# Kernel tuning notes

Hardware: AMD Instinct MI355X
Metric: run time of the kernel (lower is better)

The kernel has to match this reference:

```python
import jax, jax.numpy as jnp
import numpy as np

N = 100000      # nodes
E = 1600000     # nnz of precomputed A^K (avg degree 16)
D = 64          # in_feats
C = 64          # n_classes
LN_EPS = 1e-5


def setup_inputs() -> dict:
    key = jax.random.key(0)
    ks = jax.random.split(key, 8)
    feat = jax.random.normal(ks[0], (N, D), dtype=jnp.float32)
    feat_ori = jax.random.normal(ks[1], (N, D), dtype=jnp.float32)
    row = jax.random.randint(ks[2], (E,), 0, N)
    col = jax.random.randint(ks[3], (E,), 0, N)
    adj_vals = jax.random.uniform(ks[4], (E,), dtype=jnp.float32)
    # Linear params (xavier_uniform weight, zero bias)
    limit = float(np.sqrt(6.0 / (D + C)))
    W = jax.random.uniform(ks[5], (C, D), dtype=jnp.float32, minval=-limit, maxval=limit)
    b = jnp.zeros((C,), dtype=jnp.float32)
    # LayerNorm params
    gamma = jnp.ones((C,), dtype=jnp.float32)
    beta = jnp.zeros((C,), dtype=jnp.float32)
    return {"feat": feat, "feat_ori": feat_ori, "row": row, "col": col,
            "adj_vals": adj_vals, "W": W, "b": b, "gamma": gamma, "beta": beta}


def reference(feat, feat_ori, row, col, adj_vals, W, b, gamma, beta):
    # NOTE: in the source, h = (1-alpha)*feat + alpha*feat_ori is dead code
    # (immediately overwritten by the SpMM of raw feat), so it is omitted.
    # SpMM: h[i] = sum_{e: row[e]=i} adj_vals[e] * feat[col[e]]   -> [N, D]
    msgs = adj_vals[:, None] * feat[col]            # [E, D] gather + scale
    h = jax.ops.segment_sum(msgs, row, num_segments=N)  # [N, D] scatter-add
    # Dense Linear: [N, D] @ [D, C] + [C]
    h = jnp.einsum('nd,cd->nc', h, W) + b
    # LayerNorm over last dim
    mu = jnp.mean(h, axis=-1, keepdims=True)
    var = jnp.mean(jnp.square(h - mu), axis=-1, keepdims=True)
    h = (h - mu) * jax.lax.rsqrt(var + LN_EPS) * gamma + beta
    return h
```

## Files before the change

kernel.cpp:

```cpp
#include <hip/hip_runtime.h>


typedef unsigned int u32;
typedef unsigned short u16;
typedef unsigned long long u64;
#define RFL(x) __builtin_amdgcn_readfirstlane(x)

#define EPB 2048
#define MAXBK 2048
#define CAP 2048

__device__ __forceinline__ float bf2f(u16 v) {
    return __uint_as_float((u32)v << 16);
}
__device__ __forceinline__ u16 f2bf(float f) {
    u32 b = __float_as_uint(f);
    return (u16)((b + 0x7FFFu + ((b >> 16) & 1u)) >> 16);
}

__global__ __launch_bounds__(256) void k_bhist(const int* __restrict__ row,
                                               u32* __restrict__ hist2d,
                                               int E, int NBK) {
    __shared__ u32 cnt[MAXBK];
    for (int i = threadIdx.x; i < NBK; i += 256) cnt[i] = 0;
    __syncthreads();
    int e0 = blockIdx.x * EPB;
#pragma unroll
    for (int j = 0; j < EPB / 256; ++j) {
        int e = e0 + j * 256 + threadIdx.x;
        if (e < E) atomicAdd(&cnt[(u32)row[e] >> 6], 1u);
    }
    __syncthreads();
    u32* dst = hist2d + (size_t)blockIdx.x * NBK;
    for (int i = threadIdx.x; i < NBK; i += 256) dst[i] = cnt[i];
}

__device__ __forceinline__ u32 blk_scan256(u32 v, u32* wsum, u32& total) {
    int lane = threadIdx.x & 63, wid = threadIdx.x >> 6;
    u32 incl = v;
#pragma unroll
    for (int o = 1; o < 64; o <<= 1) {
        u32 u = __shfl_up(incl, o);
        if (lane >= o) incl += u;
    }
    if (lane == 63) wsum[wid] = incl;
    __syncthreads();
    u32 woff = 0;
    for (int w = 0; w < wid; ++w) woff += wsum[w];
    total = wsum[0] + wsum[1] + wsum[2] + wsum[3];
    __syncthreads();
    return woff + incl - v;
}

__global__ __launch_bounds__(256) void k_bscan(u32* __restrict__ hist2d,
                                               u32* __restrict__ btot,
                                               int NBLK, int NBK) {
    __shared__ u32 wsum[4];
    int bkt = blockIdx.x;
    u32 carry = 0;
    for (int r = 0; r < NBLK; r += 256) {
        int blk = r + threadIdx.x;
        u32 v = (blk < NBLK) ? hist2d[(size_t)blk * NBK + bkt] : 0;
        u32 tot;
        u32 ex = blk_scan256(v, wsum, tot);
        if (blk < NBLK) hist2d[(size_t)blk * NBK + bkt] = ex + carry;
        carry += tot;
    }
    if (threadIdx.x == 0) btot[bkt] = carry;
}

__global__ __launch_bounds__(256) void k_scanb2(const u32* __restrict__ btot,
                                                u32* __restrict__ bbase,
                                                int NBK, int E) {
    __shared__ u32 wsum[4];
    u32 carry = 0;
    for (int r = 0; r < NBK; r += 256) {
        int i = r + threadIdx.x;
        u32 v = (i < NBK) ? btot[i] : 0;
        u32 tot;
        u32 ex = blk_scan256(v, wsum, tot);
        if (i < NBK) bbase[i] = ex + carry;
        carry += tot;
    }
    if (threadIdx.x == 0) bbase[NBK] = (u32)E;
}

__global__ __launch_bounds__(256) void k_bscat(const int* __restrict__ row,
                                               const int* __restrict__ col,
                                               const float* __restrict__ vals,
                                               const u32* __restrict__ hist2d,
                                               const u32* __restrict__ bbase,
                                               u64* __restrict__ epair1,
                                               int E, int NBK) {
    __shared__ u32 lbase[MAXBK];
    __shared__ u32 lcnt[MAXBK];
    const u32* hrow = hist2d + (size_t)blockIdx.x * NBK;
    for (int i = threadIdx.x; i < NBK; i += 256) {
        lbase[i] = bbase[i] + hrow[i];
        lcnt[i] = 0;
    }
    __syncthreads();
    int e0 = blockIdx.x * EPB;
#pragma unroll
    for (int j = 0; j < EPB / 256; ++j) {
        int e = e0 + j * 256 + threadIdx.x;
        if (e < E) {
            u32 r = (u32)row[e];
            u32 bkt = r >> 6;
            u32 lrank = atomicAdd(&lcnt[bkt], 1u);
            u32 pos = lbase[bkt] + lrank;
            u32 meta = (u32)col[e] | ((r & 63u) << 26);
            epair1[pos] = (u64)meta | ((u64)__float_as_uint(vals[e]) << 32);
        }
    }
}

__global__ __launch_bounds__(256) void k_gemm(const float* __restrict__ feat,
                                              const float* __restrict__ W,
                                              u16* __restrict__ G, int N) {
    __shared__ float fs[4096];
    int lane = threadIdx.x & 63, wid = threadIdx.x >> 6;
    int n0 = blockIdx.x * 64;
    int valid = N - n0; if (valid > 64) valid = 64;
    int elems = valid * 64;
    for (int idx = threadIdx.x * 4; idx < elems; idx += 1024)
        *reinterpret_cast<float4*>(&fs[idx]) =
            *reinterpret_cast<const float4*>(&feat[(size_t)n0 * 64 + idx]);
    float wr[64];
#pragma unroll
    for (int d4 = 0; d4 < 16; ++d4) {
        float4 w4 = *reinterpret_cast<const float4*>(&W[lane * 64 + d4 * 4]);
        wr[d4 * 4 + 0] = w4.x; wr[d4 * 4 + 1] = w4.y;
        wr[d4 * 4 + 2] = w4.z; wr[d4 * 4 + 3] = w4.w;
    }
    __syncthreads();
    for (int j = 0; j < 16; ++j) {
        int r = wid * 16 + j;
        if (r >= valid) break;
        float o = 0.f;
#pragma unroll
        for (int d4 = 0; d4 < 16; ++d4) {
            float4 h4 = *reinterpret_cast<const float4*>(&fs[r * 64 + d4 * 4]);
            o = fmaf(h4.x, wr[d4 * 4 + 0], o);
            o = fmaf(h4.y, wr[d4 * 4 + 1], o);
            o = fmaf(h4.z, wr[d4 * 4 + 2], o);
            o = fmaf(h4.w, wr[d4 * 4 + 3], o);
        }
        G[(size_t)(n0 + r) * 64 + lane] = f2bf(o);
    }
}

__global__ __launch_bounds__(256) void k_node2(
    const u16* __restrict__ G, const u64* __restrict__ epair1,
    const u32* __restrict__ bbase, const float* __restrict__ bias,
    const float* __restrict__ gamma, const float* __restrict__ beta,
    float* __restrict__ out, int N)
{
    __shared__ u64 sp[CAP];
    __shared__ u32 cnt[64], base[64], cnt2[64];
    int tid = threadIdx.x, lane = tid & 63, wid = tid >> 6;
    int bkt = blockIdx.x;
    if (tid < 64) { cnt[tid] = 0; cnt2[tid] = 0; }
    __syncthreads();
    int s = RFL((int)bbase[bkt]);
    int t = RFL((int)bbase[bkt + 1]);
    int m = t - s;
    bool fits = (m <= CAP);

    const u32* meta1 = (const u32*)epair1;
    for (int i = s + tid; i < t; i += 256)
        atomicAdd(&cnt[meta1[2 * (size_t)i] >> 26], 1u);
    __syncthreads();
    if (tid < 64) {
        u32 v = cnt[tid];
        u32 incl = v;
#pragma unroll
        for (int o = 1; o < 64; o <<= 1) {
            u32 u = __shfl_up(incl, o);
            if (tid >= o) incl += u;
        }
        base[tid] = incl - v;
    }
    __syncthreads();
    if (fits) {
        for (int i = s + tid; i < t; i += 256) {
            u64 p = epair1[i];
            u32 mm = (u32)p;
            u32 r = mm >> 26;
            u32 rank = atomicAdd(&cnt2[r], 1u);
            sp[base[r] + rank] = (p & 0xFFFFFFFF00000000ull) | (u64)(mm & 0x03FFFFFFu);
        }
    }
    __syncthreads();

    int rbase = bkt << 6;
    for (int j = 0; j < 16; ++j) {
        int r = wid * 16 + j;
        int n = rbase + r;
        if (n >= N) break;
        float acc0 = 0.f, acc1 = 0.f;
        if (fits) {
            int e0 = base[r], e1 = base[r] + cnt[r];
            int i = e0;
            for (; i + 8 <= e1; i += 8) {
                u64 p0 = sp[i],     p1 = sp[i + 1];
                u64 p2 = sp[i + 2], p3 = sp[i + 3];
                u64 p4 = sp[i + 4], p5 = sp[i + 5];
                u64 p6 = sp[i + 6], p7 = sp[i + 7];
                u32 c0 = RFL((u32)p0), b0 = RFL((u32)(p0 >> 32));
                u32 c1 = RFL((u32)p1), b1 = RFL((u32)(p1 >> 32));
                u32 c2 = RFL((u32)p2), b2 = RFL((u32)(p2 >> 32));
                u32 c3 = RFL((u32)p3), b3 = RFL((u32)(p3 >> 32));
                u32 c4 = RFL((u32)p4), b4 = RFL((u32)(p4 >> 32));
                u32 c5 = RFL((u32)p5), b5 = RFL((u32)(p5 >> 32));
                u32 c6 = RFL((u32)p6), b6 = RFL((u32)(p6 >> 32));
                u32 c7 = RFL((u32)p7), b7 = RFL((u32)(p7 >> 32));
                float g0 = bf2f(G[((size_t)c0 << 6) | lane]);
                float g1 = bf2f(G[((size_t)c1 << 6) | lane]);
                float g2 = bf2f(G[((size_t)c2 << 6) | lane]);
                float g3 = bf2f(G[((size_t)c3 << 6) | lane]);
                float g4 = bf2f(G[((size_t)c4 << 6) | lane]);
                float g5 = bf2f(G[((size_t)c5 << 6) | lane]);
                float g6 = bf2f(G[((size_t)c6 << 6) | lane]);
                float g7 = bf2f(G[((size_t)c7 << 6) | lane]);
                acc0 = fmaf(__uint_as_float(b0), g0, acc0);
                acc1 = fmaf(__uint_as_float(b1), g1, acc1);
                acc0 = fmaf(__uint_as_float(b2), g2, acc0);
                acc1 = fmaf(__uint_as_float(b3), g3, acc1);
                acc0 = fmaf(__uint_as_float(b4), g4, acc0);
                acc1 = fmaf(__uint_as_float(b5), g5, acc1);
                acc0 = fmaf(__uint_as_float(b6), g6, acc0);
                acc1 = fmaf(__uint_as_float(b7), g7, acc1);
            }
            for (; i < e1; ++i) {
                u64 p = sp[i];
                u32 c = RFL((u32)p), b = RFL((u32)(p >> 32));
                acc0 = fmaf(__uint_as_float(b), bf2f(G[((size_t)c << 6) | lane]), acc0);
            }
        } else {
            for (int i = s; i < t; ++i) {
                u64 p = epair1[i];
                u32 mm = RFL((u32)p);
                if ((int)(mm >> 26) == r) {
                    u32 b = RFL((u32)(p >> 32));
                    acc0 = fmaf(__uint_as_float(b),
                                bf2f(G[((size_t)(mm & 0x03FFFFFFu) << 6) | lane]), acc0);
                }
            }
        }
        float o = acc0 + acc1 + bias[lane];

        float ssum = o;
#pragma unroll
        for (int off = 32; off; off >>= 1) ssum += __shfl_xor(ssum, off);
        float mu = ssum * 0.015625f;
        float dv = o - mu;
        float vs = dv * dv;
#pragma unroll
        for (int off = 32; off; off >>= 1) vs += __shfl_xor(vs, off);
        float inv = rsqrtf(vs * 0.015625f + 1e-5f);
        out[((size_t)n << 6) + lane] = dv * inv * gamma[lane] + beta[lane];
    }
}

extern "C" void kernel_launch(void* const* d_in, const int* in_sizes, int n_in,
                              void* d_out, int out_size, void* d_ws, size_t ws_size,
                              hipStream_t stream) {
    const float* feat  = (const float*)d_in[0];
    const int*   row   = (const int*)d_in[2];
    const int*   col   = (const int*)d_in[3];
    const float* vals  = (const float*)d_in[4];
    const float* W     = (const float*)d_in[5];
    const float* bias  = (const float*)d_in[6];
    const float* gamma = (const float*)d_in[7];
    const float* beta  = (const float*)d_in[8];
    float* out = (float*)d_out;

    const int D = 64;
    int N = in_sizes[0] / D;
    int E = in_sizes[2];

    int NBK  = (N + 63) / 64;
    int NBLK = (E + EPB - 1) / EPB;

    char* ws = (char*)d_ws;
    u16*   G      = (u16*)ws;
    u32*   hist2d = (u32*)ws;
    size_t sizeA  = (size_t)N * 128;
    size_t hsize  = (size_t)NBLK * NBK * 4;
    if (hsize > sizeA) sizeA = hsize;
    size_t boffB  = (sizeA + 255) & ~(size_t)255;
    u64*   epair1 = (u64*)(ws + boffB);
    size_t boffC  = boffB + (((size_t)E * 8 + 255) & ~(size_t)255);
    u32*   btot   = (u32*)(ws + boffC);
    u32*   bbase  = btot + NBK;

    k_bhist <<<NBLK, 256, 0, stream>>>(row, hist2d, E, NBK);
    k_bscan <<<NBK, 256, 0, stream>>>(hist2d, btot, NBLK, NBK);
    k_scanb2<<<1, 256, 0, stream>>>(btot, bbase, NBK, E);
    k_bscat <<<NBLK, 256, 0, stream>>>(row, col, vals, hist2d, bbase,
                                       epair1, E, NBK);
    k_gemm  <<<(N + 63) / 64, 256, 0, stream>>>(feat, W, G, N);
    k_node2 <<<NBK, 256, 0, stream>>>(G, epair1, bbase, bias, gamma, beta,
                                      out, N);
}
```

Before: 162.2 us.

## Shrink histogram block count and fuse edge scatter with dense GEMM launch

New measurement: 130.2 us. -19.7%, faster.

```diff
diff --git a/kernel.cpp b/kernel.cpp
--- a/kernel.cpp
+++ b/kernel.cpp
@@ -6,7 +6,7 @@
 typedef unsigned long long u64;
 #define RFL(x) __builtin_amdgcn_readfirstlane(x)
 
-#define EPB 2048
+#define NBLKC 64
 #define MAXBK 2048
 #define CAP 2048
 
@@ -20,19 +20,25 @@
 
 __global__ __launch_bounds__(256) void k_bhist(const int* __restrict__ row,
                                                u32* __restrict__ hist2d,
-                                               int E, int NBK) {
+                                               int E, int NBK, int CH) {
     __shared__ u32 cnt[MAXBK];
-    for (int i = threadIdx.x; i < NBK; i += 256) cnt[i] = 0;
-    __syncthreads();
-    int e0 = blockIdx.x * EPB;
-#pragma unroll
-    for (int j = 0; j < EPB / 256; ++j) {
-        int e = e0 + j * 256 + threadIdx.x;
-        if (e < E) atomicAdd(&cnt[(u32)row[e] >> 6], 1u);
-    }
+    int tid = threadIdx.x;
+    for (int i = tid; i < NBK; i += 256) cnt[i] = 0;
+    __syncthreads();
+    int e0 = blockIdx.x * CH;
+    int e1 = e0 + CH; if (e1 > E) e1 = E;
+    int ev = e1 & ~3;
+    for (int i = e0 + tid * 4; i < ev; i += 1024) {
+        int4 r = *reinterpret_cast<const int4*>(&row[i]);
+        atomicAdd(&cnt[(u32)r.x >> 6], 1u);
+        atomicAdd(&cnt[(u32)r.y >> 6], 1u);
+        atomicAdd(&cnt[(u32)r.z >> 6], 1u);
+        atomicAdd(&cnt[(u32)r.w >> 6], 1u);
+    }
+    { int i = ev + tid; if (i < e1) atomicAdd(&cnt[(u32)row[i] >> 6], 1u); }
     __syncthreads();
     u32* dst = hist2d + (size_t)blockIdx.x * NBK;
-    for (int i = threadIdx.x; i < NBK; i += 256) dst[i] = cnt[i];
+    for (int i = tid; i < NBK; i += 256) dst[i] = cnt[i];
 }
 
 __device__ __forceinline__ u32 blk_scan256(u32 v, u32* wsum, u32& total) {
@@ -85,68 +91,88 @@
     if (threadIdx.x == 0) bbase[NBK] = (u32)E;
 }
 
-__global__ __launch_bounds__(256) void k_bscat(const int* __restrict__ row,
-                                               const int* __restrict__ col,
-                                               const float* __restrict__ vals,
-                                               const u32* __restrict__ hist2d,
-                                               const u32* __restrict__ bbase,
-                                               u64* __restrict__ epair1,
-                                               int E, int NBK) {
-    __shared__ u32 lbase[MAXBK];
-    __shared__ u32 lcnt[MAXBK];
-    const u32* hrow = hist2d + (size_t)blockIdx.x * NBK;
-    for (int i = threadIdx.x; i < NBK; i += 256) {
-        lbase[i] = bbase[i] + hrow[i];
-        lcnt[i] = 0;
-    }
-    __syncthreads();
-    int e0 = blockIdx.x * EPB;
-#pragma unroll
-    for (int j = 0; j < EPB / 256; ++j) {
-        int e = e0 + j * 256 + threadIdx.x;
-        if (e < E) {
-            u32 r = (u32)row[e];
-            u32 bkt = r >> 6;
-            u32 lrank = atomicAdd(&lcnt[bkt], 1u);
-            u32 pos = lbase[bkt] + lrank;
-            u32 meta = (u32)col[e] | ((r & 63u) << 26);
-            epair1[pos] = (u64)meta | ((u64)__float_as_uint(vals[e]) << 32);
-        }
-    }
-}
-
-__global__ __launch_bounds__(256) void k_gemm(const float* __restrict__ feat,
-                                              const float* __restrict__ W,
-                                              u16* __restrict__ G, int N) {
-    __shared__ float fs[4096];
-    int lane = threadIdx.x & 63, wid = threadIdx.x >> 6;
-    int n0 = blockIdx.x * 64;
-    int valid = N - n0; if (valid > 64) valid = 64;
-    int elems = valid * 64;
-    for (int idx = threadIdx.x * 4; idx < elems; idx += 1024)
-        *reinterpret_cast<float4*>(&fs[idx]) =
-            *reinterpret_cast<const float4*>(&feat[(size_t)n0 * 64 + idx]);
-    float wr[64];
-#pragma unroll
-    for (int d4 = 0; d4 < 16; ++d4) {
-        float4 w4 = *reinterpret_cast<const float4*>(&W[lane * 64 + d4 * 4]);
-        wr[d4 * 4 + 0] = w4.x; wr[d4 * 4 + 1] = w4.y;
-        wr[d4 * 4 + 2] = w4.z; wr[d4 * 4 + 3] = w4.w;
-    }
-    __syncthreads();
-    for (int j = 0; j < 16; ++j) {
-        int r = wid * 16 + j;
-        if (r >= valid) break;
-        float o = 0.f;
+__global__ __launch_bounds__(256) void k_scatgemm(
+    const int* __restrict__ row, const int* __restrict__ col,
+    const float* __restrict__ vals, const u32* __restrict__ hist2d,
+    const u32* __restrict__ bbase, u64* __restrict__ epair1,
+    const float* __restrict__ feat, const float* __restrict__ W,
+    u16* __restrict__ G, int E, int N, int NBK, int NBLK, int CH)
+{
+    __shared__ __align__(16) u32 smem[4096];
+    int tid = threadIdx.x;
+    if ((int)blockIdx.x < NBLK) {
+        u32* lbase = smem;
+        u32* lcnt  = smem + NBK;
+        int blk = blockIdx.x;
+        const u32* hrow = hist2d + (size_t)blk * NBK;
+        for (int i = tid; i < NBK; i += 256) {
+            lbase[i] = bbase[i] + hrow[i];
+            lcnt[i] = 0;
+        }
+        __syncthreads();
+        int e0 = blk * CH;
+        int e1 = e0 + CH; if (e1 > E) e1 = E;
+        int ev = e1 & ~3;
+        for (int i = e0 + tid * 4; i < ev; i += 1024) {
+            int4 r = *reinterpret_cast<const int4*>(&row[i]);
+            int4 c = *reinterpret_cast<const int4*>(&col[i]);
+            float4 v = *reinterpret_cast<const float4*>(&vals[i]);
+            u32 k0 = (u32)r.x >> 6, k1 = (u32)r.y >> 6;
+            u32 k2 = (u32)r.z >> 6, k3 = (u32)r.w >> 6;
+            u32 q0 = atomicAdd(&lcnt[k0], 1u);
+            u32 q1 = atomicAdd(&lcnt[k1], 1u);
+            u32 q2 = atomicAdd(&lcnt[k2], 1u);
+            u32 q3 = atomicAdd(&lcnt[k3], 1u);
+            epair1[lbase[k0] + q0] = (u64)((u32)c.x | (((u32)r.x & 63u) << 26))
+                                   | ((u64)__float_as_uint(v.x) << 32);
+            epair1[lbase[k1] + q1] = (u64)((u32)c.y | (((u32)r.y & 63u) << 26))
+                                   | ((u64)__float_as_uint(v.y) << 32);
+            epair1[lbase[k2] + q2] = (u64)((u32)c.z | (((u32)r.z & 63u) << 26))
+                                   | ((u64)__float_as_uint(v.z) << 32);
+            epair1[lbase[k3] + q3] = (u64)((u32)c.w | (((u32)r.w & 63u) << 26))
+                                   | ((u64)__float_as_uint(v.w) << 32);
+        }
+        {
+            int i = ev + tid;
+            if (i < e1) {
+                u32 r = (u32)row[i];
+                u32 k = r >> 6;
+                u32 q = atomicAdd(&lcnt[k], 1u);
+                epair1[lbase[k] + q] = (u64)((u32)col[i] | ((r & 63u) << 26))
+                                     | ((u64)__float_as_uint(vals[i]) << 32);
+            }
+        }
+    } else {
+        float* fs = (float*)smem;
+        int lane = tid & 63, wid = tid >> 6;
+        int n0 = ((int)blockIdx.x - NBLK) * 64;
+        int valid = N - n0; if (valid > 64) valid = 64;
+        int elems = valid * 64;
+        for (int idx = tid * 4; idx < elems; idx += 1024)
+            *reinterpret_cast<float4*>(&fs[idx]) =
+                *reinterpret_cast<const float4*>(&feat[(size_t)n0 * 64 + idx]);
+        float wr[64];
 #pragma unroll
         for (int d4 = 0; d4 < 16; ++d4) {
-            float4 h4 = *reinterpret_cast<const float4*>(&fs[r * 64 + d4 * 4]);
-            o = fmaf(h4.x, wr[d4 * 4 + 0], o);
-            o = fmaf(h4.y, wr[d4 * 4 + 1], o);
-            o = fmaf(h4.z, wr[d4 * 4 + 2], o);
-            o = fmaf(h4.w, wr[d4 * 4 + 3], o);
-        }
-        G[(size_t)(n0 + r) * 64 + lane] = f2bf(o);
+            float4 w4 = *reinterpret_cast<const float4*>(&W[lane * 64 + d4 * 4]);
+            wr[d4 * 4 + 0] = w4.x; wr[d4 * 4 + 1] = w4.y;
+            wr[d4 * 4 + 2] = w4.z; wr[d4 * 4 + 3] = w4.w;
+        }
+        __syncthreads();
+        for (int j = 0; j < 16; ++j) {
+            int r = wid * 16 + j;
+            if (r >= valid) break;
+            float o = 0.f;
+#pragma unroll
+            for (int d4 = 0; d4 < 16; ++d4) {
+                float4 h4 = *reinterpret_cast<const float4*>(&fs[r * 64 + d4 * 4]);
+                o = fmaf(h4.x, wr[d4 * 4 + 0], o);
+                o = fmaf(h4.y, wr[d4 * 4 + 1], o);
+                o = fmaf(h4.z, wr[d4 * 4 + 2], o);
+                o = fmaf(h4.w, wr[d4 * 4 + 3], o);
+            }
+            G[(size_t)(n0 + r) * 64 + lane] = f2bf(o);
+        }
     }
 }
 
@@ -281,26 +307,26 @@
     int E = in_sizes[2];
 
     int NBK  = (N + 63) / 64;
-    int NBLK = (E + EPB - 1) / EPB;
+    int NBLK = NBLKC;
+    int CH   = (((E + NBLK - 1) / NBLK) + 3) & ~3;
+    int NG   = (N + 63) / 64;
 
     char* ws = (char*)d_ws;
     u16*   G      = (u16*)ws;
-    u32*   hist2d = (u32*)ws;
-    size_t sizeA  = (size_t)N * 128;
-    size_t hsize  = (size_t)NBLK * NBK * 4;
-    if (hsize > sizeA) sizeA = hsize;
-    size_t boffB  = (sizeA + 255) & ~(size_t)255;
-    u64*   epair1 = (u64*)(ws + boffB);
-    size_t boffC  = boffB + (((size_t)E * 8 + 255) & ~(size_t)255);
-    u32*   btot   = (u32*)(ws + boffC);
+    size_t off1   = (((size_t)N * 128) + 255) & ~(size_t)255;
+    u64*   epair1 = (u64*)(ws + off1);
+    size_t off2   = off1 + (((size_t)E * 8 + 255) & ~(size_t)255);
+    u32*   hist2d = (u32*)(ws + off2);
+    size_t off3   = off2 + (((size_t)NBLK * NBK * 4 + 255) & ~(size_t)255);
+    u32*   btot   = (u32*)(ws + off3);
     u32*   bbase  = btot + NBK;
 
-    k_bhist <<<NBLK, 256, 0, stream>>>(row, hist2d, E, NBK);
-    k_bscan <<<NBK, 256, 0, stream>>>(hist2d, btot, NBLK, NBK);
-    k_scanb2<<<1, 256, 0, stream>>>(btot, bbase, NBK, E);
-    k_bscat <<<NBLK, 256, 0, stream>>>(row, col, vals, hist2d, bbase,
-                                       epair1, E, NBK);
-    k_gemm  <<<(N + 63) / 64, 256, 0, stream>>>(feat, W, G, N);
-    k_node2 <<<NBK, 256, 0, stream>>>(G, epair1, bbase, bias, gamma, beta,
-                                      out, N);
-}
+    k_bhist   <<<NBLK, 256, 0, stream>>>(row, hist2d, E, NBK, CH);
+    k_bscan   <<<NBK, 256, 0, stream>>>(hist2d, btot, NBLK, NBK);
+    k_scanb2  <<<1, 256, 0, stream>>>(btot, bbase, NBK, E);
+    k_scatgemm<<<NBLK + NG, 256, 0, stream>>>(row, col, vals, hist2d, bbase,
+                                              epair1, feat, W, G,
+                                              E, N, NBK, NBLK, CH);
+    k_node2   <<<NBK, 256, 0, stream>>>(G, epair1, bbase, bias, gamma, beta,
+                                        out, N);
+}
```
